# Kernel optimization log

Hardware: AMD Instinct MI355X
Metric: run time of the kernel (lower is better)

Reference implementation:

```python
import jax, jax.numpy as jnp
import numpy as np

N_NODES = 100000
N_EDGES = 1600000
IN = 128
OUT = 32
HEADS = 4
NEG_SLOPE = 0.2


def setup_inputs() -> dict:
    key = jax.random.key(0)
    ks = jax.random.split(key, 6)
    x = jax.random.normal(ks[0], (N_NODES, IN), dtype=jnp.float32)
    row = jax.random.randint(ks[1], (N_EDGES,), 0, N_NODES, dtype=jnp.int32)
    col = jax.random.randint(ks[2], (N_EDGES,), 0, N_NODES, dtype=jnp.int32)
    W = jax.random.normal(ks[3], (OUT * HEADS, IN), dtype=jnp.float32) * (1.0 / np.sqrt(IN))
    b = jnp.zeros((OUT * HEADS,), dtype=jnp.float32)
    a_l = jax.random.normal(ks[4], (1, OUT, HEADS), dtype=jnp.float32) * 0.1
    a_r = jax.random.normal(ks[5], (1, OUT, HEADS), dtype=jnp.float32) * 0.1
    return {"x": x, "row": row, "col": col, "W": W, "b": b, "a_l": a_l, "a_r": a_r}


def reference(x, row, col, W, b, a_l, a_r):
    N = x.shape[0]
    # Z: [N, OUT, HEADS] (row-major view of [N, OUT*HEADS], matching torch .view)
    Z = (x @ W.T + b).reshape(N, OUT, HEADS)
    e_l = jnp.sum(Z * a_l, axis=1)  # [N, HEADS]
    e_r = jnp.sum(Z * a_r, axis=1)  # [N, HEADS]
    e = e_l[row] + e_r[col]         # [E, HEADS]
    e = jnp.where(e > 0, e, NEG_SLOPE * e)  # LeakyReLU
    # segment softmax over edges grouped by destination (row)
    m = jax.ops.segment_max(e, row, num_segments=N)      # [N, HEADS]
    ex = jnp.exp(e - m[row])                              # [E, HEADS]
    denom = jax.ops.segment_sum(ex, row, num_segments=N)  # [N, HEADS]
    alpha = ex / denom[row]                               # [E, HEADS]
    # bspmm: out[i,:,h] = sum_{(i,j) in E} alpha[e,h] * Z[j,:,h]
    out = jax.ops.segment_sum(alpha[:, None, :] * Z[col], row, num_segments=N)
    return out
```

## Files before the change

kernel.cpp:

```cpp
#include <hip/hip_runtime.h>
#include <hip/hip_bf16.h>
#include <math.h>


typedef __attribute__((ext_vector_type(8))) short bf16x8;
typedef __attribute__((ext_vector_type(4))) float f32x4;

__device__ __forceinline__ ushort f2bf(float f) {
  __hip_bfloat16 h = __float2bfloat16(f);
  return __builtin_bit_cast(ushort, h);
}
__device__ __forceinline__ float bf2f(ushort u) {
  unsigned v = ((unsigned)u) << 16;
  return __builtin_bit_cast(float, v);
}

__global__ __launch_bounds__(256) void prep_w(
    const float* __restrict__ W, ushort* __restrict__ Wh,
    ushort* __restrict__ Wl) {
  int i = blockIdx.x * 256 + threadIdx.x;
  float w = W[i];
  ushort hb = f2bf(w);
  Wh[i] = hb;
  Wl[i] = f2bf(w - bf2f(hb));
}

__global__ __launch_bounds__(512, 4) void gemm_z(
    const float* __restrict__ x, const ushort* __restrict__ Wh,
    const ushort* __restrict__ Wl, const float* __restrict__ bias,
    ushort* __restrict__ Zh, int N) {
  __shared__ ushort xh[64 * 128];
  __shared__ ushort xl[64 * 128];
  const int t = threadIdx.x;
  const int lane = t & 63;
  const int wv = t >> 6;
  const int row0 = blockIdx.x * 64;
  const int l15 = lane & 15, l4 = lane >> 4;
  const int ch = wv * 16 + l15;

  bf16x8 Bh[4], Bl[4];
#pragma unroll
  for (int kf = 0; kf < 4; ++kf) {
    int off = ch * 128 + kf * 32 + l4 * 8;
    Bh[kf] = *(const bf16x8*)&Wh[off];
    Bl[kf] = *(const bf16x8*)&Wl[off];
  }

#pragma unroll
  for (int i = 0; i < 4; ++i) {
    int f4 = i * 512 + t;
    int r = f4 >> 5;
    int k = (f4 & 31) * 4;
    int gr = row0 + r;
    float4 v = make_float4(0.f, 0.f, 0.f, 0.f);
    if (gr < N) v = ((const float4*)x)[(size_t)gr * 32 + (f4 & 31)];
    float vf[4] = {v.x, v.y, v.z, v.w};
    ushort hs[4], ls[4];
#pragma unroll
    for (int j = 0; j < 4; ++j) {
      hs[j] = f2bf(vf[j]);
      ls[j] = f2bf(vf[j] - bf2f(hs[j]));
    }
    int idx = r * 128 + (k ^ ((r & 7) << 3));
    uint2 hv, lv;
    hv.x = hs[0] | ((unsigned)hs[1] << 16);
    hv.y = hs[2] | ((unsigned)hs[3] << 16);
    lv.x = ls[0] | ((unsigned)ls[1] << 16);
    lv.y = ls[2] | ((unsigned)ls[3] << 16);
    *(uint2*)&xh[idx] = hv;
    *(uint2*)&xl[idx] = lv;
  }
  __syncthreads();

  f32x4 acc[4];
#pragma unroll
  for (int rt = 0; rt < 4; ++rt) acc[rt] = (f32x4){0.f, 0.f, 0.f, 0.f};

#pragma unroll
  for (int kf = 0; kf < 4; ++kf) {
#pragma unroll
    for (int rt = 0; rt < 4; ++rt) {
      int r = rt * 16 + l15;
      int idx = r * 128 + ((kf * 32 + l4 * 8) ^ ((r & 7) << 3));
      bf16x8 ah = *(const bf16x8*)&xh[idx];
      bf16x8 al = *(const bf16x8*)&xl[idx];
      acc[rt] = __builtin_amdgcn_mfma_f32_16x16x32_bf16(ah, Bh[kf], acc[rt], 0, 0, 0);
      acc[rt] = __builtin_amdgcn_mfma_f32_16x16x32_bf16(al, Bh[kf], acc[rt], 0, 0, 0);
      acc[rt] = __builtin_amdgcn_mfma_f32_16x16x32_bf16(ah, Bl[kf], acc[rt], 0, 0, 0);
    }
  }

  float bv = bias[ch];
  unsigned zc = (unsigned)((ch & 3) * 32 + (ch >> 2));
#pragma unroll
  for (int rt = 0; rt < 4; ++rt) {
#pragma unroll
    for (int j = 0; j < 4; ++j) {
      int r = row0 + rt * 16 + l4 * 4 + j;
      if (r < N) Zh[(unsigned)r * 128 + zc] = f2bf(acc[rt][j] + bv);
    }
  }
}

__global__ __launch_bounds__(256) void deg_cnt(
    const int* __restrict__ row, int* __restrict__ deg,
    int* __restrict__ rank, int E) {
  int e = blockIdx.x * 256 + threadIdx.x;
  if (e < E) rank[e] = atomicAdd(&deg[row[e]], 1);
}

__global__ __launch_bounds__(256) void node_scan(
    const ushort* __restrict__ Zh, const float* __restrict__ a_l,
    const float* __restrict__ a_r, float* __restrict__ el,
    float* __restrict__ er, int N4,
    const int* __restrict__ deg, int* __restrict__ basev,
    int* __restrict__ bsum, int N, int G1) {
  __shared__ float sal[128], sar[128];
  __shared__ int ss[256];
  int t = threadIdx.x;

  if ((int)blockIdx.x < G1) {
    if (t < 128) { sal[t] = a_l[t]; sar[t] = a_r[t]; }
    __syncthreads();
    int idx = blockIdx.x * 256 + t;
    if (idx >= N4) return;
    int n = idx >> 2, h = idx & 3;
    const ushort* zp = Zh + (unsigned)n * 128 + h * 32;
    float sl = 0.f, sr = 0.f;
#pragma unroll
    for (int q = 0; q < 8; ++q) {
      uint2 zz = *(const uint2*)&zp[q * 4];
      float z0 = bf2f((ushort)(zz.x & 0xffff));
      float z1 = bf2f((ushort)(zz.x >> 16));
      float z2 = bf2f((ushort)(zz.y & 0xffff));
      float z3 = bf2f((ushort)(zz.y >> 16));
      int o = q * 4;
      sl += z0 * sal[(o + 0) * 4 + h] + z1 * sal[(o + 1) * 4 + h]
          + z2 * sal[(o + 2) * 4 + h] + z3 * sal[(o + 3) * 4 + h];
      sr += z0 * sar[(o + 0) * 4 + h] + z1 * sar[(o + 1) * 4 + h]
          + z2 * sar[(o + 2) * 4 + h] + z3 * sar[(o + 3) * 4 + h];
    }
    el[idx] = sl;
    er[idx] = sr;
  } else {
    int bid = (int)blockIdx.x - G1;
    int i = bid * 256 + t;
    int v = (i < N) ? deg[i] : 0;
    ss[t] = v;
    __syncthreads();
#pragma unroll
    for (int off = 1; off < 256; off <<= 1) {
      int u = (t >= off) ? ss[t - off] : 0;
      __syncthreads();
      ss[t] += u;
      __syncthreads();
    }
    if (i < N) basev[i] = ss[t] - v;
    if (t == 255) bsum[bid] = ss[255];
  }
}

__global__ __launch_bounds__(512) void scan2(int* __restrict__ bsum, int NB) {
  __shared__ int s[512];
  int v = (threadIdx.x < NB) ? bsum[threadIdx.x] : 0;
  s[threadIdx.x] = v;
  __syncthreads();
#pragma unroll
  for (int off = 1; off < 512; off <<= 1) {
    int t = (threadIdx.x >= off) ? s[threadIdx.x - off] : 0;
    __syncthreads();
    s[threadIdx.x] += t;
    __syncthreads();
  }
  if (threadIdx.x < NB) bsum[threadIdx.x] = s[threadIdx.x] - v;
}

__global__ __launch_bounds__(256) void fill(
    const int* __restrict__ row, const int* __restrict__ col,
    const int* __restrict__ rank, const int* __restrict__ base,
    const int* __restrict__ bsum, int* __restrict__ sorted_col, int E) {
  int e = blockIdx.x * 256 + threadIdx.x;
  if (e < E) {
    int r = row[e];
    sorted_col[base[r] + bsum[r >> 8] + rank[e]] = col[e];
  }
}

__global__ __launch_bounds__(256) void gather(
    const int* __restrict__ base, const int* __restrict__ bsum,
    const int* __restrict__ deg, const int* __restrict__ sorted_col,
    const float* __restrict__ el, const float* __restrict__ er,
    const ushort* __restrict__ Zh, float* __restrict__ out, int N) {
  int t = threadIdx.x;
  int lane = t & 63;
  int n = blockIdx.x * 4 + (t >> 6);
  if (n >= N) return;
  int h = lane >> 4;
  int j = lane & 15;
  int s = base[n] + bsum[n >> 8];
  int d = deg[n];
  int end = s + d;
  float elv = el[((unsigned)n << 2) + h];
  float acc0 = 0.f, acc1 = 0.f, sumA = 0.f;
  const unsigned* Zh32 = (const unsigned*)Zh;
  const unsigned zlane = (unsigned)lane;
  const int bpb = (lane & 48) << 2;

  for (int p = s; p < end; p += 16) {
    int cnt = end - p;
    int cl6 = 0;
    float xv = 0.f;
    if (j < cnt) {
      int cl = sorted_col[p + j];
      float e = elv + er[((unsigned)cl << 2) + h];
      e = fmaxf(e, 0.2f * e);
      xv = __expf(e);
      cl6 = cl << 6;
    }
    sumA += xv;
    float xvb[16];
    unsigned addr[16];
#pragma unroll
    for (int jj = 0; jj < 16; ++jj) {
      int a = bpb + (jj << 2);
      xvb[jj] = __builtin_bit_cast(float,
          __builtin_amdgcn_ds_bpermute(a, __builtin_bit_cast(int, xv)));
      addr[jj] = (unsigned)__builtin_amdgcn_ds_bpermute(a, cl6) + zlane;
    }
    unsigned zz[16];
#pragma unroll
    for (int jj = 0; jj < 16; ++jj) zz[jj] = Zh32[addr[jj]];
#pragma unroll
    for (int jj = 0; jj < 16; ++jj) {
      acc0 = fmaf(xvb[jj], __builtin_bit_cast(float, zz[jj] << 16), acc0);
      acc1 = fmaf(xvb[jj], __builtin_bit_cast(float, zz[jj] & 0xffff0000u), acc1);
    }
  }
  float sum = sumA;
  sum += __shfl_xor(sum, 1, 64);
  sum += __shfl_xor(sum, 2, 64);
  sum += __shfl_xor(sum, 4, 64);
  sum += __shfl_xor(sum, 8, 64);
  float inv = (d > 0) ? 1.0f / sum : 0.f;
  unsigned o0 = (unsigned)(j << 1);
  unsigned ob = ((unsigned)n << 7) + (o0 << 2) + (unsigned)h;
  out[ob] = acc0 * inv;
  out[ob + 4] = acc1 * inv;
}

extern "C" void kernel_launch(void* const* d_in, const int* in_sizes, int n_in,
                              void* d_out, int out_size, void* d_ws, size_t ws_size,
                              hipStream_t stream) {
  const float* x   = (const float*)d_in[0];
  const int*   row = (const int*)d_in[1];
  const int*   col = (const int*)d_in[2];
  const float* W   = (const float*)d_in[3];
  const float* b   = (const float*)d_in[4];
  const float* a_l = (const float*)d_in[5];
  const float* a_r = (const float*)d_in[6];
  float* out = (float*)d_out;

  const int N = in_sizes[0] / 128;
  const int E = in_sizes[1];
  const int NB = (N + 255) / 256;

  char* w = (char*)d_ws;
  ushort* Zh       = (ushort*)w;             w += (size_t)N * 128 * 2;
  int*   sorted_col= (int*)w;                w += (size_t)E * 4;
  int*   rank      = (int*)w;                w += (size_t)E * 4;
  float* el        = (float*)w;              w += (size_t)N * 4 * 4;
  float* er        = (float*)w;              w += (size_t)N * 4 * 4;
  int*   deg       = (int*)w;                w += (size_t)N * 4;
  int*   base      = (int*)w;                w += (size_t)N * 4;
  int*   bsum      = (int*)w;                w += 512 * 4;
  ushort* Wh       = (ushort*)w;             w += 16384 * 2;
  ushort* Wl       = (ushort*)w;             w += 16384 * 2;

  hipMemsetAsync(deg, 0, (size_t)N * sizeof(int), stream);

  prep_w<<<64, 256, 0, stream>>>(W, Wh, Wl);
  deg_cnt<<<(E + 255) / 256, 256, 0, stream>>>(row, deg, rank, E);
  gemm_z<<<(N + 63) / 64, 512, 0, stream>>>(x, Wh, Wl, b, Zh, N);

  const int G1n = (N * 4 + 255) / 256;
  node_scan<<<G1n + NB, 256, 0, stream>>>(Zh, a_l, a_r, el, er, N * 4,
                                          deg, base, bsum, N, G1n);
  scan2<<<1, 512, 0, stream>>>(bsum, NB);
  fill<<<(E + 255) / 256, 256, 0, stream>>>(row, col, rank, base, bsum,
                                            sorted_col, E);
  gather<<<(N + 3) / 4, 256, 0, stream>>>(base, bsum, deg, sorted_col, el, er,
                                          Zh, out, N);
}
```

Baseline: 220.2 us.

## Interleave Z layout so gather writes output coalesced, stage Z stores via LDS

Changes the bf16 Z storage layout so that each 32-bit word pairs output features o and o+16 for the same head, interleaved by head. The gather kernel then maps lanes so that each thread's two accumulators land on contiguous output addresses, written with nontemporal stores instead of strided scattered writes. The GEMM epilogue stages Z through LDS and writes full 128-element rows with 16-byte stores instead of scattered 2-byte stores, and node_scan is adapted to the new layout. This adds an extra LDS round trip and two barriers in the GEMM.

```diff
diff --git a/kernel.cpp b/kernel.cpp
--- a/kernel.cpp
+++ b/kernel.cpp
@@ -29,8 +29,10 @@
     const float* __restrict__ x, const ushort* __restrict__ Wh,
     const ushort* __restrict__ Wl, const float* __restrict__ bias,
     ushort* __restrict__ Zh, int N) {
-  __shared__ ushort xh[64 * 128];
-  __shared__ ushort xl[64 * 128];
+  __shared__ __align__(16) ushort smem[16384];
+  ushort* xh = smem;
+  ushort* xl = smem + 8192;
+  ushort* zs = smem;
   const int t = threadIdx.x;
   const int lane = t & 63;
   const int wv = t >> 6;
@@ -89,15 +91,31 @@
       acc[rt] = __builtin_amdgcn_mfma_f32_16x16x32_bf16(ah, Bl[kf], acc[rt], 0, 0, 0);
     }
   }
-
-  float bv = bias[ch];
-  unsigned zc = (unsigned)((ch & 3) * 32 + (ch >> 2));
-#pragma unroll
-  for (int rt = 0; rt < 4; ++rt) {
-#pragma unroll
-    for (int j = 0; j < 4; ++j) {
-      int r = row0 + rt * 16 + l4 * 4 + j;
-      if (r < N) Zh[(unsigned)r * 128 + zc] = f2bf(acc[rt][j] + bv);
+  __syncthreads();
+
+  {
+    float bv = bias[ch];
+    int o = ch >> 2, h = ch & 3;
+    int s = (o & 15) * 8 + h * 2 + (o >> 4);
+#pragma unroll
+    for (int rt = 0; rt < 4; ++rt) {
+#pragma unroll
+      for (int j = 0; j < 4; ++j) {
+        int r = rt * 16 + l4 * 4 + j;
+        zs[r * 132 + s] = f2bf(acc[rt][j] + bv);
+      }
+    }
+  }
+  __syncthreads();
+  {
+    int r = t >> 3;
+    int c = t & 7;
+    int gr = row0 + r;
+    if (gr < N) {
+      uint4 v0 = *(const uint4*)&zs[r * 132 + c * 16];
+      uint4 v1 = *(const uint4*)&zs[r * 132 + c * 16 + 8];
+      *(uint4*)&Zh[(size_t)gr * 128 + c * 16] = v0;
+      *(uint4*)&Zh[(size_t)gr * 128 + c * 16 + 8] = v1;
     }
   }
 }
@@ -125,20 +143,16 @@
     int idx = blockIdx.x * 256 + t;
     if (idx >= N4) return;
     int n = idx >> 2, h = idx & 3;
-    const ushort* zp = Zh + (unsigned)n * 128 + h * 32;
+    const unsigned* zp = (const unsigned*)Zh + (unsigned)n * 64 + h;
     float sl = 0.f, sr = 0.f;
 #pragma unroll
-    for (int q = 0; q < 8; ++q) {
-      uint2 zz = *(const uint2*)&zp[q * 4];
-      float z0 = bf2f((ushort)(zz.x & 0xffff));
-      float z1 = bf2f((ushort)(zz.x >> 16));
-      float z2 = bf2f((ushort)(zz.y & 0xffff));
-      float z3 = bf2f((ushort)(zz.y >> 16));
-      int o = q * 4;
-      sl += z0 * sal[(o + 0) * 4 + h] + z1 * sal[(o + 1) * 4 + h]
-          + z2 * sal[(o + 2) * 4 + h] + z3 * sal[(o + 3) * 4 + h];
-      sr += z0 * sar[(o + 0) * 4 + h] + z1 * sar[(o + 1) * 4 + h]
-          + z2 * sar[(o + 2) * 4 + h] + z3 * sar[(o + 3) * 4 + h];
+    for (int o = 0; o < 16; ++o) {
+      unsigned zz = zp[o * 4];
+      float zlo = bf2f((ushort)(zz & 0xffff));
+      float zhi = bf2f((ushort)(zz >> 16));
+      int c = (o << 2) + h;
+      sl += zlo * sal[c] + zhi * sal[c + 64];
+      sr += zlo * sar[c] + zhi * sar[c + 64];
     }
     el[idx] = sl;
     er[idx] = sr;
@@ -195,8 +209,8 @@
   int lane = t & 63;
   int n = blockIdx.x * 4 + (t >> 6);
   if (n >= N) return;
-  int h = lane >> 4;
-  int j = lane & 15;
+  int h = lane & 3;
+  int jj = lane >> 2;
   int s = base[n] + bsum[n >> 8];
   int d = deg[n];
   int end = s + d;
@@ -204,14 +218,14 @@
   float acc0 = 0.f, acc1 = 0.f, sumA = 0.f;
   const unsigned* Zh32 = (const unsigned*)Zh;
   const unsigned zlane = (unsigned)lane;
-  const int bpb = (lane & 48) << 2;
+  const int bpb = (lane & 3) << 2;
 
   for (int p = s; p < end; p += 16) {
     int cnt = end - p;
     int cl6 = 0;
     float xv = 0.f;
-    if (j < cnt) {
-      int cl = sorted_col[p + j];
+    if (jj < cnt) {
+      int cl = sorted_col[p + jj];
       float e = elv + er[((unsigned)cl << 2) + h];
       e = fmaxf(e, 0.2f * e);
       xv = __expf(e);
@@ -221,31 +235,30 @@
     float xvb[16];
     unsigned addr[16];
 #pragma unroll
-    for (int jj = 0; jj < 16; ++jj) {
-      int a = bpb + (jj << 2);
-      xvb[jj] = __builtin_bit_cast(float,
+    for (int q = 0; q < 16; ++q) {
+      int a = bpb + (q << 4);
+      xvb[q] = __builtin_bit_cast(float,
           __builtin_amdgcn_ds_bpermute(a, __builtin_bit_cast(int, xv)));
-      addr[jj] = (unsigned)__builtin_amdgcn_ds_bpermute(a, cl6) + zlane;
+      addr[q] = (unsigned)__builtin_amdgcn_ds_bpermute(a, cl6) + zlane;
     }
     unsigned zz[16];
 #pragma unroll
-    for (int jj = 0; jj < 16; ++jj) zz[jj] = Zh32[addr[jj]];
-#pragma unroll
-    for (int jj = 0; jj < 16; ++jj) {
-      acc0 = fmaf(xvb[jj], __builtin_bit_cast(float, zz[jj] << 16), acc0);
-      acc1 = fmaf(xvb[jj], __builtin_bit_cast(float, zz[jj] & 0xffff0000u), acc1);
+    for (int q = 0; q < 16; ++q) zz[q] = Zh32[addr[q]];
+#pragma unroll
+    for (int q = 0; q < 16; ++q) {
+      acc0 = fmaf(xvb[q], __builtin_bit_cast(float, zz[q] << 16), acc0);
+      acc1 = fmaf(xvb[q], __builtin_bit_cast(float, zz[q] & 0xffff0000u), acc1);
     }
   }
   float sum = sumA;
-  sum += __shfl_xor(sum, 1, 64);
-  sum += __shfl_xor(sum, 2, 64);
   sum += __shfl_xor(sum, 4, 64);
   sum += __shfl_xor(sum, 8, 64);
+  sum += __shfl_xor(sum, 16, 64);
+  sum += __shfl_xor(sum, 32, 64);
   float inv = (d > 0) ? 1.0f / sum : 0.f;
-  unsigned o0 = (unsigned)(j << 1);
-  unsigned ob = ((unsigned)n << 7) + (o0 << 2) + (unsigned)h;
-  out[ob] = acc0 * inv;
-  out[ob + 4] = acc1 * inv;
+  unsigned ob = ((unsigned)n << 7) + zlane;
+  __builtin_nontemporal_store(acc0 * inv, &out[ob]);
+  __builtin_nontemporal_store(acc1 * inv, &out[ob + 64]);
 }
 
 extern "C" void kernel_launch(void* const* d_in, const int* in_sizes, int n_in,
```

New measurement: 211.2 us. 1.04x faster.
